# Performance work log

Measured on AMD Instinct MI355X. Metric: run time of the kernel, lower is better.

The kernel has to match this reference:

```python
import jax, jax.numpy as jnp
import numpy as np

MAXDISP = 48
GROUP = 8
EPS = 1e-5


def setup_inputs() -> dict:
    key = jax.random.key(0)
    k1, k2 = jax.random.split(key)
    x = jax.random.normal(k1, (2, 64, 96, 320), dtype=jnp.float32)
    y = jax.random.normal(k2, (2, 64, 96, 320), dtype=jnp.float32)
    return {"x": x, "y": y}


def reference(x, y):
    # Faithful translation of CostVolume.forward.
    # torch's unfold over left-zero-padded y at kernel position d picks
    # y_pad[..., j + d]; per-window L2 norm over channels reduces to a
    # per-pixel channel norm (padded zeros normalize to zero), so we
    # normalize once and gather shifted columns.
    D = MAXDISP + 1
    b, c, h, w = x.shape
    cpg = c // GROUP
    xg = x.reshape(b, GROUP, cpg, h, w)
    yg = y.reshape(b, GROUP, cpg, h, w)
    xn = xg / (jnp.linalg.norm(xg, axis=2, keepdims=True) + EPS)
    yn = yg / (jnp.linalg.norm(yg, axis=2, keepdims=True) + EPS)
    # left zero-pad width dim by MAXDISP (padded zeros stay zero after norm)
    y_pad = jnp.pad(yn, ((0, 0), (0, 0), (0, 0), (0, 0), (MAXDISP, 0)))
    # after torch.flip on the disparity axis, disparity k compares x[:, j]
    # with y[:, j - k]  ->  padded index j + MAXDISP - k
    idx = jnp.arange(w)[None, :] + MAXDISP - jnp.arange(D)[:, None]  # [D, w]
    y_shift = y_pad[..., idx]  # [b, g, cpg, h, D, w]
    cost = jnp.sum(jnp.abs(xn[:, :, :, :, None, :] - y_shift), axis=2)  # [b,g,h,D,w]
    return jnp.transpose(cost, (0, 1, 3, 2, 4))  # [b, group, D, h, w]
```

## Files before the change

### kernel.cpp

```cpp
#include <hip/hip_runtime.h>


#define MAXDISP 48
#define NDISP   49
#define HH      96
#define WW      320
#define HW      (HH * WW)
#define EPSN    1e-5f

__global__ __launch_bounds__(320) void cost_volume_kernel(
    const float* __restrict__ x, const float* __restrict__ y,
    float* __restrict__ out)
{
    __shared__ float4 ylds[2][2][2][WW / 2];

    const int tid = threadIdx.x;
    const int q   = tid % 160;
    const int r   = tid / 160;
    const int j   = 2 * q;

    const int blk = blockIdx.x;
    const int hp  = blk % (HH / 2);
    const int bg  = blk / (HH / 2);
    const int h   = hp * 2 + r;

    const int inBase = bg * 8 * HW + h * WW + j;

    float xa[8], xb[8], ya[8], yb[8];
    float xsa = 0.f, xsb = 0.f, ysa = 0.f, ysb = 0.f;
#pragma unroll
    for (int cc = 0; cc < 8; ++cc) {
        const float2 xi = *reinterpret_cast<const float2*>(x + inBase + cc * HW);
        const float2 yi = *reinterpret_cast<const float2*>(y + inBase + cc * HW);
        xa[cc] = xi.x; xb[cc] = xi.y;
        ya[cc] = yi.x; yb[cc] = yi.y;
        xsa += xi.x * xi.x; xsb += xi.y * xi.y;
        ysa += yi.x * yi.x; ysb += yi.y * yi.y;
    }
    const float xia = 1.f / (sqrtf(xsa) + EPSN);
    const float xib = 1.f / (sqrtf(xsb) + EPSN);
    const float yia = 1.f / (sqrtf(ysa) + EPSN);
    const float yib = 1.f / (sqrtf(ysb) + EPSN);

    float sAbsA = 0.f, sAbsB = 0.f;
#pragma unroll
    for (int cc = 0; cc < 8; ++cc) {
        xa[cc] *= xia; xb[cc] *= xib;
        ya[cc] *= yia; yb[cc] *= yib;
        sAbsA += fabsf(xa[cc]);
        sAbsB += fabsf(xb[cc]);
    }

    ylds[r][0][0][q] = make_float4(ya[0], ya[1], ya[2], ya[3]);
    ylds[r][0][1][q] = make_float4(ya[4], ya[5], ya[6], ya[7]);
    ylds[r][1][0][q] = make_float4(yb[0], yb[1], yb[2], yb[3]);
    ylds[r][1][1][q] = make_float4(yb[4], yb[5], yb[6], yb[7]);
    __syncthreads();

    const float4* ldsE = &ylds[r][0][0][0];
    const float4* ldsO = &ylds[r][1][0][0];

    float4 yp0 = ldsE[q],       yp1 = ldsE[160 + q];
    float4 yc0 = ldsO[q],       yc1 = ldsO[160 + q];

    const float4* bcur = ldsO;
    const float4* bnxt = ldsE;

    float* outp = out + bg * (NDISP * HW) + h * WW + j;

#pragma unroll 7
    for (int d = 0; d < NDISP; ++d) {
        float c0 = fabsf(xa[0] - yp0.x) + fabsf(xa[1] - yp0.y)
                 + fabsf(xa[2] - yp0.z) + fabsf(xa[3] - yp0.w)
                 + fabsf(xa[4] - yp1.x) + fabsf(xa[5] - yp1.y)
                 + fabsf(xa[6] - yp1.z) + fabsf(xa[7] - yp1.w);
        float c1 = fabsf(xb[0] - yc0.x) + fabsf(xb[1] - yc0.y)
                 + fabsf(xb[2] - yc0.z) + fabsf(xb[3] - yc0.w)
                 + fabsf(xb[4] - yc1.x) + fabsf(xb[5] - yc1.y)
                 + fabsf(xb[6] - yc1.z) + fabsf(xb[7] - yc1.w);
        c0 = (d <= j)     ? c0 : sAbsA;
        c1 = (d <= j + 1) ? c1 : sAbsB;
        *reinterpret_cast<float2*>(outp) = make_float2(c0, c1);
        outp += HW;

        yc0 = yp0; yc1 = yp1;
        const int pn  = j - d - 1;
        const int idx = (pn > 0 ? pn : 0) >> 1;
        yp0 = bcur[idx];
        yp1 = bcur[160 + idx];
        const float4* t = bcur; bcur = bnxt; bnxt = t;
    }
}

extern "C" void kernel_launch(void* const* d_in, const int* in_sizes, int n_in,
                              void* d_out, int out_size, void* d_ws, size_t ws_size,
                              hipStream_t stream) {
    const float* x = (const float*)d_in[0];
    const float* y = (const float*)d_in[1];
    float* out = (float*)d_out;
    dim3 grid(2 * 8 * (HH / 2));
    dim3 block(320);
    cost_volume_kernel<<<grid, block, 0, stream>>>(x, y, out);
}
```

Baseline: 132.9 us.

## Split disparity range across thread halves, one row per block

Each block now processes a single image row, with the two halves of the block covering disparities 0–24 and 24–48 instead of two different rows. The shifted y row is normalized once into shared memory by half the threads, and the disparity loop is fully unrolled with compile-time buffer selection. The grid doubles and launch bounds request higher occupancy, aiming to shorten the serial per-thread chain and expose more parallelism. Disparity 24 is computed and written redundantly by both halves.

```diff
diff --git a/kernel.cpp b/kernel.cpp
--- a/kernel.cpp
+++ b/kernel.cpp
@@ -8,88 +8,102 @@
 #define HW      (HH * WW)
 #define EPSN    1e-5f
 
-__global__ __launch_bounds__(320) void cost_volume_kernel(
+__global__ __launch_bounds__(320, 8) void cost_volume_kernel(
     const float* __restrict__ x, const float* __restrict__ y,
     float* __restrict__ out)
 {
-    __shared__ float4 ylds[2][2][2][WW / 2];
+    __shared__ float4 ylds[2][2][WW / 2];
 
-    const int tid = threadIdx.x;
-    const int q   = tid % 160;
-    const int r   = tid / 160;
-    const int j   = 2 * q;
+    const int tid   = threadIdx.x;
+    const int q     = tid % 160;
+    const int r     = tid / 160;
+    const int j     = 2 * q;
+    const int dbase = 24 * r;
 
     const int blk = blockIdx.x;
-    const int hp  = blk % (HH / 2);
-    const int bg  = blk / (HH / 2);
-    const int h   = hp * 2 + r;
+    const int h   = blk % HH;
+    const int bg  = blk / HH;
 
     const int inBase = bg * 8 * HW + h * WW + j;
 
-    float xa[8], xb[8], ya[8], yb[8];
-    float xsa = 0.f, xsb = 0.f, ysa = 0.f, ysb = 0.f;
+    float xa[8], xb[8];
+    float xsa = 0.f, xsb = 0.f;
 #pragma unroll
     for (int cc = 0; cc < 8; ++cc) {
         const float2 xi = *reinterpret_cast<const float2*>(x + inBase + cc * HW);
-        const float2 yi = *reinterpret_cast<const float2*>(y + inBase + cc * HW);
         xa[cc] = xi.x; xb[cc] = xi.y;
-        ya[cc] = yi.x; yb[cc] = yi.y;
         xsa += xi.x * xi.x; xsb += xi.y * xi.y;
-        ysa += yi.x * yi.x; ysb += yi.y * yi.y;
     }
     const float xia = 1.f / (sqrtf(xsa) + EPSN);
     const float xib = 1.f / (sqrtf(xsb) + EPSN);
-    const float yia = 1.f / (sqrtf(ysa) + EPSN);
-    const float yib = 1.f / (sqrtf(ysb) + EPSN);
-
     float sAbsA = 0.f, sAbsB = 0.f;
 #pragma unroll
     for (int cc = 0; cc < 8; ++cc) {
         xa[cc] *= xia; xb[cc] *= xib;
-        ya[cc] *= yia; yb[cc] *= yib;
         sAbsA += fabsf(xa[cc]);
         sAbsB += fabsf(xb[cc]);
     }
 
-    ylds[r][0][0][q] = make_float4(ya[0], ya[1], ya[2], ya[3]);
-    ylds[r][0][1][q] = make_float4(ya[4], ya[5], ya[6], ya[7]);
-    ylds[r][1][0][q] = make_float4(yb[0], yb[1], yb[2], yb[3]);
-    ylds[r][1][1][q] = make_float4(yb[4], yb[5], yb[6], yb[7]);
+    if (tid < 160) {
+        float ya[8], yb[8];
+        float ysa = 0.f, ysb = 0.f;
+#pragma unroll
+        for (int cc = 0; cc < 8; ++cc) {
+            const float2 yi = *reinterpret_cast<const float2*>(y + inBase + cc * HW);
+            ya[cc] = yi.x; yb[cc] = yi.y;
+            ysa += yi.x * yi.x; ysb += yi.y * yi.y;
+        }
+        const float yia = 1.f / (sqrtf(ysa) + EPSN);
+        const float yib = 1.f / (sqrtf(ysb) + EPSN);
+#pragma unroll
+        for (int cc = 0; cc < 8; ++cc) { ya[cc] *= yia; yb[cc] *= yib; }
+        ylds[0][0][q] = make_float4(ya[0], ya[1], ya[2], ya[3]);
+        ylds[0][1][q] = make_float4(ya[4], ya[5], ya[6], ya[7]);
+        ylds[1][0][q] = make_float4(yb[0], yb[1], yb[2], yb[3]);
+        ylds[1][1][q] = make_float4(yb[4], yb[5], yb[6], yb[7]);
+    }
     __syncthreads();
 
-    const float4* ldsE = &ylds[r][0][0][0];
-    const float4* ldsO = &ylds[r][1][0][0];
+    const float4* const ldsE = &ylds[0][0][0];
+    const float4* const ldsO = &ylds[1][0][0];
 
-    float4 yp0 = ldsE[q],       yp1 = ldsE[160 + q];
-    float4 yc0 = ldsO[q],       yc1 = ldsO[160 + q];
+    const int p0  = j - dbase;
+    const int ix0 = (p0 > 0 ? p0 : 0) >> 1;
+    float4 yp0 = ldsE[ix0], yp1 = ldsE[160 + ix0];
+    float4 yc0 = ldsO[ix0], yc1 = ldsO[160 + ix0];
 
-    const float4* bcur = ldsO;
-    const float4* bnxt = ldsE;
+    float* const outBase = out + bg * (NDISP * HW) + h * WW + j;
 
-    float* outp = out + bg * (NDISP * HW) + h * WW + j;
+#define CV_STEP(D, FB, DO_FRESH)                                            \
+    {                                                                       \
+        float c0 = fabsf(xa[0] - yp0.x) + fabsf(xa[1] - yp0.y)              \
+                 + fabsf(xa[2] - yp0.z) + fabsf(xa[3] - yp0.w)              \
+                 + fabsf(xa[4] - yp1.x) + fabsf(xa[5] - yp1.y)              \
+                 + fabsf(xa[6] - yp1.z) + fabsf(xa[7] - yp1.w);             \
+        float c1 = fabsf(xb[0] - yc0.x) + fabsf(xb[1] - yc0.y)              \
+                 + fabsf(xb[2] - yc0.z) + fabsf(xb[3] - yc0.w)              \
+                 + fabsf(xb[4] - yc1.x) + fabsf(xb[5] - yc1.y)              \
+                 + fabsf(xb[6] - yc1.z) + fabsf(xb[7] - yc1.w);             \
+        c0 = ((D) <= j)     ? c0 : sAbsA;                                   \
+        c1 = ((D) <= j + 1) ? c1 : sAbsB;                                   \
+        *reinterpret_cast<float2*>(outBase + (D) * HW) = make_float2(c0, c1);\
+        yc0 = yp0; yc1 = yp1;                                               \
+        if (DO_FRESH) {                                                     \
+            const int pn = j - (D) - 1;                                     \
+            const int ix = (pn > 0 ? pn : 0) >> 1;                          \
+            yp0 = (FB)[ix]; yp1 = (FB)[160 + ix];                           \
+        }                                                                   \
+    }
 
-#pragma unroll 7
-    for (int d = 0; d < NDISP; ++d) {
-        float c0 = fabsf(xa[0] - yp0.x) + fabsf(xa[1] - yp0.y)
-                 + fabsf(xa[2] - yp0.z) + fabsf(xa[3] - yp0.w)
-                 + fabsf(xa[4] - yp1.x) + fabsf(xa[5] - yp1.y)
-                 + fabsf(xa[6] - yp1.z) + fabsf(xa[7] - yp1.w);
-        float c1 = fabsf(xb[0] - yc0.x) + fabsf(xb[1] - yc0.y)
-                 + fabsf(xb[2] - yc0.z) + fabsf(xb[3] - yc0.w)
-                 + fabsf(xb[4] - yc1.x) + fabsf(xb[5] - yc1.y)
-                 + fabsf(xb[6] - yc1.z) + fabsf(xb[7] - yc1.w);
-        c0 = (d <= j)     ? c0 : sAbsA;
-        c1 = (d <= j + 1) ? c1 : sAbsB;
-        *reinterpret_cast<float2*>(outp) = make_float2(c0, c1);
-        outp += HW;
+#pragma unroll
+    for (int ii = 0; ii < 12; ++ii) {
+        const int d0 = dbase + 2 * ii;
+        CV_STEP(d0,     ldsO, 1);
+        CV_STEP(d0 + 1, ldsE, 1);
+    }
+    CV_STEP(dbase + 24, ldsO, 0);
 
-        yc0 = yp0; yc1 = yp1;
-        const int pn  = j - d - 1;
-        const int idx = (pn > 0 ? pn : 0) >> 1;
-        yp0 = bcur[idx];
-        yp1 = bcur[160 + idx];
-        const float4* t = bcur; bcur = bnxt; bnxt = t;
-    }
+#undef CV_STEP
 }
 
 extern "C" void kernel_launch(void* const* d_in, const int* in_sizes, int n_in,
@@ -98,7 +112,7 @@
     const float* x = (const float*)d_in[0];
     const float* y = (const float*)d_in[1];
     float* out = (float*)d_out;
-    dim3 grid(2 * 8 * (HH / 2));
-    dim3 block(320);
+    dim3 grid(2 * 8 * HH);
+    dim3 block(WW);
     cost_volume_kernel<<<grid, block, 0, stream>>>(x, y, out);
 }
```

Measured after the change: 158.4 us. 19.2% more time.
